# Performance work log

Hardware: AMD Instinct MI355X
Metric: run time of the kernel (lower is better)

The kernel has to match this reference:

```python
import jax, jax.numpy as jnp
import numpy as np

D = 64        # dense voxel grid extent per axis
C = 256       # planes
R = 128       # planes // reduction
N = 100000    # number of occupied (unique) sparse voxels
K = 7         # max-pool kernel size
PAD = 3       # (K-1)//2, stride-1 'same' window


def setup_inputs() -> dict:
    key = jax.random.key(0)
    k1, k2, k3, k4 = jax.random.split(key, 4)
    feats = jax.random.normal(k1, (N, C), dtype=jnp.float32)
    # unique sparse coordinates in [0, D)^3 (MinkowskiEngine coords are unique)
    lin = jax.random.permutation(k2, D * D * D)[:N]
    coords = jnp.stack(jnp.unravel_index(lin, (D, D, D)), axis=-1).astype(jnp.int32)
    # 1x1 sparse convs == per-point linear layers (ME default bias=False)
    W1 = jax.random.normal(k3, (C, R), dtype=jnp.float32) * (1.0 / np.sqrt(C))
    W2 = jax.random.normal(k4, (R, C), dtype=jnp.float32) * (1.0 / np.sqrt(R))
    return {"feats": feats, "coords": coords, "W1": W1, "W2": W2}


def reference(feats, coords, W1, W2):
    neg_inf = jnp.array(-jnp.inf, dtype=feats.dtype)
    ix, iy, iz = coords[:, 0], coords[:, 1], coords[:, 2]
    # scatter sparse features into a dense grid; empty voxels = -inf so they
    grid = jnp.full((D, D, D, C), neg_inf, dtype=feats.dtype).at[ix, iy, iz].set(feats)
    # MinkowskiMaxPooling(kernel_size=7, stride=1): max over [-3,3]^3 window
    pooled = jax.lax.reduce_window(
        grid, neg_inf, jax.lax.max,
        window_dimensions=(K, K, K, 1),
        window_strides=(1, 1, 1, 1),
        padding=[(PAD, PAD), (PAD, PAD), (PAD, PAD), (0, 0)],
    )
    y = pooled[ix, iy, iz]  # [N, C], gather back to sparse points
    # fc: 1x1 conv -> ReLU -> 1x1 conv -> sigmoid (per-point MLP)
    y = jax.nn.sigmoid(jax.nn.relu(y @ W1) @ W2)
    return feats * y
```

## Files before the change

kernel.cpp:

```cpp
#include <hip/hip_runtime.h>
#include <hip/hip_bf16.h>

#define GD 64
#define GC 256

typedef unsigned short u16;
typedef unsigned int u32;
typedef short bf16x8 __attribute__((ext_vector_type(8)));
typedef float f32x4 __attribute__((ext_vector_type(4)));

__device__ __forceinline__ u16 f2bf_rne(float f) {
    u32 u = __builtin_bit_cast(u32, f);
    u = (u + 0x7FFFu + ((u >> 16) & 1u)) >> 16;
    return (u16)u;
}

__device__ __forceinline__ float bfval(float f) {
    u32 u = __builtin_bit_cast(u32, f);
    u = (u + 0x7FFFu + ((u >> 16) & 1u)) & 0xFFFF0000u;
    return __builtin_bit_cast(float, u);
}

__device__ __forceinline__ void unpack8(uint4 r, float* w) {
    u32 v[4] = {r.x, r.y, r.z, r.w};
#pragma unroll
    for (int i = 0; i < 4; i++) {
        w[2 * i]     = __builtin_bit_cast(float, v[i] << 16);
        w[2 * i + 1] = __builtin_bit_cast(float, v[i] & 0xFFFF0000u);
    }
}

__global__ __launch_bounds__(256) void init_map(uint4* __restrict__ m) {
    int i = blockIdx.x * 256 + threadIdx.x;
    uint4 v;
    v.x = v.y = v.z = v.w = 0xFFFFFFFFu;
    m[i] = v;
}

__global__ __launch_bounds__(256) void build_map(const int* __restrict__ coords,
        int* __restrict__ map, int n) {
    int i = blockIdx.x * 256 + threadIdx.x;
    if (i < n) {
        int ix = coords[3 * i], iy = coords[3 * i + 1], iz = coords[3 * i + 2];
        map[(ix * GD + iy) * GD + iz] = i;
    }
}

__global__ __launch_bounds__(256) void pool_z_gather(const float* __restrict__ feats,
        const int* __restrict__ map, u16* __restrict__ grid) {
    int chunk = threadIdx.x & 31;
    int L = blockIdx.x * 8 + (threadIdx.x >> 5);
    const int* mrow = map + L * GD;
    u16* p = grid + (size_t)L * GD * GC + chunk * 8;

    float win[7][8];
#pragma unroll
    for (int s = 0; s < 7; s++)
#pragma unroll
        for (int cc = 0; cc < 8; cc++) win[s][cc] = -INFINITY;

#pragma unroll
    for (int t = 0; t < 3; t++) {
        int mi = mrow[t];
        if (mi >= 0) {
            const float4* f4 = (const float4*)(feats + (size_t)mi * GC + chunk * 8);
            float4 a = f4[0], b = f4[1];
            win[t + 3][0] = bfval(a.x); win[t + 3][1] = bfval(a.y);
            win[t + 3][2] = bfval(a.z); win[t + 3][3] = bfval(a.w);
            win[t + 3][4] = bfval(b.x); win[t + 3][5] = bfval(b.y);
            win[t + 3][6] = bfval(b.z); win[t + 3][7] = bfval(b.w);
        }
    }

#pragma unroll
    for (int z = 0; z < 64; z++) {
        int slot = (z + 6) % 7;
        bool live = false;
        if (z + 3 < 64) {
            int mi = mrow[z + 3];
            if (mi >= 0) {
                live = true;
                const float4* f4 = (const float4*)(feats + (size_t)mi * GC + chunk * 8);
                float4 a = f4[0], b = f4[1];
                win[slot][0] = bfval(a.x); win[slot][1] = bfval(a.y);
                win[slot][2] = bfval(a.z); win[slot][3] = bfval(a.w);
                win[slot][4] = bfval(b.x); win[slot][5] = bfval(b.y);
                win[slot][6] = bfval(b.z); win[slot][7] = bfval(b.w);
            }
        }
        if (!live) {
#pragma unroll
            for (int cc = 0; cc < 8; cc++) win[slot][cc] = -INFINITY;
        }
        u32 q[4];
#pragma unroll
        for (int i = 0; i < 4; i++) {
            u32 halves[2];
#pragma unroll
            for (int hh = 0; hh < 2; hh++) {
                int c = 2 * i + hh;
                float m01 = fmaxf(win[0][c], win[1][c]);
                float m23 = fmaxf(win[2][c], win[3][c]);
                float m45 = fmaxf(win[4][c], win[5][c]);
                float m = fmaxf(fmaxf(m01, m23), fmaxf(m45, win[6][c]));
                halves[hh] = __builtin_bit_cast(u32, m);
            }
            q[i] = (halves[0] >> 16) | (halves[1] & 0xFFFF0000u);
        }
        *(uint4*)(p + (size_t)z * GC) = make_uint4(q[0], q[1], q[2], q[3]);
    }
}

__global__ __launch_bounds__(256) void pool_pass_v(u16* __restrict__ grid,
        int mulA, int mulB, int strideCell) {
    int chunk = threadIdx.x & 31;
    int L = blockIdx.x * 8 + (threadIdx.x >> 5);
    int a = L >> 6, b = L & 63;
    size_t baseEl = ((size_t)a * mulA + (size_t)b * mulB) * GC + chunk * 8;
    size_t stepEl = (size_t)strideCell * GC;
    u16* p = grid + baseEl;

    float win[7][8];
#pragma unroll
    for (int s = 0; s < 7; s++)
#pragma unroll
        for (int c = 0; c < 8; c++) win[s][c] = -INFINITY;

#pragma unroll
    for (int t = 0; t < 3; t++) {
        uint4 r = *(const uint4*)(p + (size_t)t * stepEl);
        unpack8(r, win[t + 3]);
    }

#pragma unroll
    for (int z = 0; z < 64; z++) {
        int slot = (z + 6) % 7;
        if (z + 3 < 64) {
            uint4 r = *(const uint4*)(p + (size_t)(z + 3) * stepEl);
            unpack8(r, win[slot]);
        } else {
#pragma unroll
            for (int c = 0; c < 8; c++) win[slot][c] = -INFINITY;
        }
        u32 q[4];
#pragma unroll
        for (int i = 0; i < 4; i++) {
            u32 halves[2];
#pragma unroll
            for (int hh = 0; hh < 2; hh++) {
                int c = 2 * i + hh;
                float m01 = fmaxf(win[0][c], win[1][c]);
                float m23 = fmaxf(win[2][c], win[3][c]);
                float m45 = fmaxf(win[4][c], win[5][c]);
                float m = fmaxf(fmaxf(m01, m23), fmaxf(m45, win[6][c]));
                halves[hh] = __builtin_bit_cast(u32, m);
            }
            q[i] = (halves[0] >> 16) | (halves[1] & 0xFFFF0000u);
        }
        *(uint4*)(p + (size_t)z * stepEl) = make_uint4(q[0], q[1], q[2], q[3]);
    }
}

__global__ __launch_bounds__(256) void pool_x_compact(const u16* __restrict__ grid,
        const int* __restrict__ map, u16* __restrict__ P) {
    int chunk = threadIdx.x & 31;
    int L = blockIdx.x * 8 + (threadIdx.x >> 5);
    int cellBase = L;
    const u16* p = grid + (size_t)cellBase * GC + chunk * 8;
    size_t stepEl = (size_t)(GD * GD) * GC;

    float win[7][8];
#pragma unroll
    for (int s = 0; s < 7; s++)
#pragma unroll
        for (int cc = 0; cc < 8; cc++) win[s][cc] = -INFINITY;

#pragma unroll
    for (int t = 0; t < 3; t++) {
        uint4 r = *(const uint4*)(p + (size_t)t * stepEl);
        unpack8(r, win[t + 3]);
    }

#pragma unroll
    for (int x = 0; x < 64; x++) {
        int slot = (x + 6) % 7;
        if (x + 3 < 64) {
            uint4 r = *(const uint4*)(p + (size_t)(x + 3) * stepEl);
            unpack8(r, win[slot]);
        } else {
#pragma unroll
            for (int cc = 0; cc < 8; cc++) win[slot][cc] = -INFINITY;
        }
        int mi = map[cellBase + x * GD * GD];
        if (mi >= 0) {
            u32 q[4];
#pragma unroll
            for (int iq = 0; iq < 4; iq++) {
                u32 halves[2];
#pragma unroll
                for (int hh = 0; hh < 2; hh++) {
                    int cc = 2 * iq + hh;
                    float m01 = fmaxf(win[0][cc], win[1][cc]);
                    float m23 = fmaxf(win[2][cc], win[3][cc]);
                    float m45 = fmaxf(win[4][cc], win[5][cc]);
                    float m = fmaxf(fmaxf(m01, m23), fmaxf(m45, win[6][cc]));
                    halves[hh] = __builtin_bit_cast(u32, m);
                }
                q[iq] = (halves[0] >> 16) | (halves[1] & 0xFFFF0000u);
            }
            *(uint4*)(P + (size_t)mi * GC + chunk * 8) = make_uint4(q[0], q[1], q[2], q[3]);
        }
    }
}

__global__ __launch_bounds__(256) void prep_weights(const float* __restrict__ W1,
        const float* __restrict__ W2, u16* __restrict__ img1, u16* __restrict__ img2) {
    int t = blockIdx.x * 256 + threadIdx.x;
    if (t < 32768) {
        int h = t >> 14, nn = (t >> 8) & 63, chunk = (t >> 3) & 31, j = t & 7;
        int k = chunk * 8 + j;
        img1[(h << 14) + nn * 256 + (((chunk ^ (nn & 7)) << 3) | j)] =
            f2bf_rne(W1[k * 128 + h * 64 + nn]);
    } else {
        int t2 = t - 32768;
        int h = t2 >> 14, nn = (t2 >> 7) & 127, chunk = (t2 >> 3) & 15, j = t2 & 7;
        int k = chunk * 8 + j;
        img2[(h << 14) + nn * 128 + (((chunk ^ (nn & 7)) << 3) | j)] =
            f2bf_rne(W2[k * 256 + h * 128 + nn]);
    }
}

__global__ __launch_bounds__(256, 4) void gemm1_kernel(const u16* __restrict__ P,
        const u16* __restrict__ img1, u16* __restrict__ H, int n, int nrb) {
    __shared__ __align__(16) u16 w1t[64 * 256];
    int h = blockIdx.x >= nrb;
    int rb = blockIdx.x - (h ? nrb : 0);
    int tid = threadIdx.x;

    const uint4* src = (const uint4*)(img1 + (h << 14));
    uint4* dst = (uint4*)w1t;
#pragma unroll
    for (int i = 0; i < 8; i++) dst[i * 256 + tid] = src[i * 256 + tid];

    int wave = tid >> 6, lane = tid & 63, m16 = lane & 15, quad = lane >> 4;
    int row_a = rb * 64 + wave * 16 + m16;
    int ra = min(row_a, n - 1);
    const u16* yrow = P + (size_t)ra * GC;
    bf16x8 afr[8];
#pragma unroll
    for (int kk = 0; kk < 8; kk++)
        afr[kk] = *(const bf16x8*)(yrow + kk * 32 + quad * 8);
    __syncthreads();

    f32x4 acc[4];
#pragma unroll
    for (int t = 0; t < 4; t++) acc[t] = (f32x4){0.f, 0.f, 0.f, 0.f};
#pragma unroll
    for (int kk = 0; kk < 8; kk++) {
        int chunk = kk * 4 + quad;
#pragma unroll
        for (int t = 0; t < 4; t++) {
            int r = t * 16 + m16;
            bf16x8 b = *(const bf16x8*)&w1t[r * 256 + ((chunk ^ (r & 7)) << 3)];
            acc[t] = __builtin_amdgcn_mfma_f32_16x16x32_bf16(afr[kk], b, acc[t], 0, 0, 0);
        }
    }
    __syncthreads();

    u16* hbuf = w1t;
#pragma unroll
    for (int t = 0; t < 4; t++) {
        int col = t * 16 + m16;
        int c8 = col >> 3, j = col & 7;
#pragma unroll
        for (int rr = 0; rr < 4; rr++) {
            int row_l = wave * 16 + quad * 4 + rr;
            float hv = fmaxf(acc[t][rr], 0.0f);
            hbuf[row_l * 64 + (((c8 ^ (row_l & 7)) << 3) | j)] = f2bf_rne(hv);
        }
    }
    __syncthreads();
#pragma unroll
    for (int i = 0; i < 2; i++) {
        int cid = i * 256 + tid;
        int row_l = cid >> 3, c8 = cid & 7;
        int grow = rb * 64 + row_l;
        if (grow < n) {
            bf16x8 v = *(const bf16x8*)&hbuf[row_l * 64 + ((c8 ^ (row_l & 7)) << 3)];
            *(bf16x8*)&H[(size_t)grow * 128 + h * 64 + c8 * 8] = v;
        }
    }
}

__global__ __launch_bounds__(256, 4) void gemm2_kernel(const u16* __restrict__ H,
        const u16* __restrict__ img2, const float* __restrict__ feats,
        float* __restrict__ out, int n, int nrb) {
    __shared__ __align__(16) char smem[64 * 140 * 4];
    u16* w2t = (u16*)smem;
    float* zbuf = (float*)smem;
    int h = blockIdx.x >= nrb;
    int rb = blockIdx.x - (h ? nrb : 0);
    int tid = threadIdx.x;

    const uint4* src = (const uint4*)(img2 + (h << 14));
    uint4* dst = (uint4*)w2t;
#pragma unroll
    for (int i = 0; i < 8; i++) dst[i * 256 + tid] = src[i * 256 + tid];

    int wave = tid >> 6, lane = tid & 63, m16 = lane & 15, quad = lane >> 4;
    int row_a = rb * 64 + wave * 16 + m16;
    int ra = min(row_a, n - 1);
    const u16* hrow = H + (size_t)ra * 128;
    bf16x8 afr[4];
#pragma unroll
    for (int kk = 0; kk < 4; kk++)
        afr[kk] = *(const bf16x8*)(hrow + kk * 32 + quad * 8);
    __syncthreads();

    f32x4 acc[8];
#pragma unroll
    for (int t = 0; t < 8; t++) acc[t] = (f32x4){0.f, 0.f, 0.f, 0.f};
#pragma unroll
    for (int kk = 0; kk < 4; kk++) {
        int chunk = kk * 4 + quad;
#pragma unroll
        for (int t = 0; t < 8; t++) {
            int nn = t * 16 + m16;
            bf16x8 b = *(const bf16x8*)&w2t[nn * 128 + ((chunk ^ (nn & 7)) << 3)];
            acc[t] = __builtin_amdgcn_mfma_f32_16x16x32_bf16(afr[kk], b, acc[t], 0, 0, 0);
        }
    }
    __syncthreads();

#pragma unroll
    for (int t = 0; t < 8; t++) {
        int col = t * 16 + m16;
#pragma unroll
        for (int rr = 0; rr < 4; rr++) {
            int row_l = wave * 16 + quad * 4 + rr;
            zbuf[row_l * 140 + col] = acc[t][rr];
        }
    }
    __syncthreads();
#pragma unroll
    for (int i = 0; i < 8; i++) {
        int f = i * 256 + tid;
        int row_l = f >> 5, c4 = f & 31;
        int grow = rb * 64 + row_l;
        if (grow < n) {
            f32x4 z = *(const f32x4*)&zbuf[row_l * 140 + c4 * 4];
            size_t o = (size_t)grow * 256 + h * 128 + c4 * 4;
            f32x4 ft = *(const f32x4*)&feats[o];
            f32x4 r;
#pragma unroll
            for (int c = 0; c < 4; c++)
                r[c] = ft[c] / (1.0f + __expf(-z[c]));
            *(f32x4*)&out[o] = r;
        }
    }
}

extern "C" void kernel_launch(void* const* d_in, const int* in_sizes, int n_in,
                              void* d_out, int out_size, void* d_ws, size_t ws_size,
                              hipStream_t stream) {
    const float* feats = (const float*)d_in[0];
    const int* coords = (const int*)d_in[1];
    const float* W1 = (const float*)d_in[2];
    const float* W2 = (const float*)d_in[3];
    float* out = (float*)d_out;

    int n = in_sizes[1] / 3;

    size_t grid_bytes = (size_t)GD * GD * GD * GC * 2;
    size_t P_bytes = (size_t)n * GC * 2;
    size_t H_bytes = (size_t)n * 128 * 2;
    u16* grid = (u16*)d_ws;
    u16* P = (u16*)((char*)d_ws + grid_bytes);
    u16* H = (u16*)((char*)d_ws + grid_bytes + P_bytes);
    int* map = (int*)((char*)d_ws + grid_bytes + P_bytes + H_bytes);
    u16* img1 = (u16*)((char*)map + (size_t)GD * GD * GD * 4);
    u16* img2 = img1 + 32768;

    init_map<<<256, 256, 0, stream>>>((uint4*)map);
    prep_weights<<<256, 256, 0, stream>>>(W1, W2, img1, img2);
    build_map<<<(n + 255) / 256, 256, 0, stream>>>(coords, map, n);

    pool_z_gather<<<512, 256, 0, stream>>>(feats, map, grid);
    pool_pass_v<<<512, 256, 0, stream>>>(grid, GD * GD, 1, GD);
    pool_x_compact<<<512, 256, 0, stream>>>(grid, map, P);

    int nrb = (n + 63) / 64;
    gemm1_kernel<<<2 * nrb, 256, 0, stream>>>(P, img1, H, n, nrb);
    gemm2_kernel<<<2 * nrb, 256, 0, stream>>>(H, img2, feats, out, n, nrb);
}
```

Measured before the change: 448.2 us.

## Split pooling lines into halves and ping-pong the y pass between grids

Each separable max-pool pass now splits every 64-long line into two 32-output halves handled by separate warps, with a 6-element halo reload. This doubles the number of blocks to raise occupancy and latency hiding. Map indices are loaded once per warp and broadcast with shuffles instead of per-iteration scalar loads. The y pass now writes to a second grid buffer instead of working in place, which avoids read/write hazards between halves but doubles workspace and adds halo re-read traffic.

Result: faster. 375.1 us (-16.3%).

```diff
diff --git a/kernel.cpp b/kernel.cpp
--- a/kernel.cpp
+++ b/kernel.cpp
@@ -28,6 +28,25 @@
         w[2 * i]     = __builtin_bit_cast(float, v[i] << 16);
         w[2 * i + 1] = __builtin_bit_cast(float, v[i] & 0xFFFF0000u);
     }
+}
+
+__device__ __forceinline__ uint4 maxpack(const float (&win)[7][8]) {
+    u32 q[4];
+#pragma unroll
+    for (int i = 0; i < 4; i++) {
+        u32 halves[2];
+#pragma unroll
+        for (int hh = 0; hh < 2; hh++) {
+            int c = 2 * i + hh;
+            float m01 = fmaxf(win[0][c], win[1][c]);
+            float m23 = fmaxf(win[2][c], win[3][c]);
+            float m45 = fmaxf(win[4][c], win[5][c]);
+            float m = fmaxf(fmaxf(m01, m23), fmaxf(m45, win[6][c]));
+            halves[hh] = __builtin_bit_cast(u32, m);
+        }
+        q[i] = (halves[0] >> 16) | (halves[1] & 0xFFFF0000u);
+    }
+    return make_uint4(q[0], q[1], q[2], q[3]);
 }
 
 __global__ __launch_bounds__(256) void init_map(uint4* __restrict__ m) {
@@ -46,171 +65,156 @@
     }
 }
 
+template<int Z0>
+__device__ __forceinline__ void pool_z_half(const float* __restrict__ fb,
+        int2 mv, u16* __restrict__ p) {
+    float win[7][8];
+#pragma unroll
+    for (int s = 0; s < 7; s++)
+#pragma unroll
+        for (int c = 0; c < 8; c++) win[s][c] = -INFINITY;
+
+#pragma unroll
+    for (int t = 0; t < 6; t++) {
+        const int w = Z0 - 3 + t;
+        if (w >= 0) {
+            int mi = __shfl((w & 1) ? mv.y : mv.x, (w >> 1) & 31, 32);
+            if (mi >= 0) {
+                const float4* f4 = (const float4*)(fb + (size_t)mi * GC);
+                float4 a = f4[0], b = f4[1];
+                float* ws = win[(w + 3) % 7];
+                ws[0] = bfval(a.x); ws[1] = bfval(a.y);
+                ws[2] = bfval(a.z); ws[3] = bfval(a.w);
+                ws[4] = bfval(b.x); ws[5] = bfval(b.y);
+                ws[6] = bfval(b.z); ws[7] = bfval(b.w);
+            }
+        }
+    }
+
+#pragma unroll
+    for (int d = 0; d < 32; d++) {
+        const int z = Z0 + d, w = z + 3, slot = (w + 3) % 7;
+        bool live = false;
+        if (w < 64) {
+            int mi = __shfl((w & 1) ? mv.y : mv.x, (w >> 1) & 31, 32);
+            if (mi >= 0) {
+                live = true;
+                const float4* f4 = (const float4*)(fb + (size_t)mi * GC);
+                float4 a = f4[0], b = f4[1];
+                float* ws = win[slot];
+                ws[0] = bfval(a.x); ws[1] = bfval(a.y);
+                ws[2] = bfval(a.z); ws[3] = bfval(a.w);
+                ws[4] = bfval(b.x); ws[5] = bfval(b.y);
+                ws[6] = bfval(b.z); ws[7] = bfval(b.w);
+            }
+        }
+        if (!live) {
+#pragma unroll
+            for (int c = 0; c < 8; c++) win[slot][c] = -INFINITY;
+        }
+        *(uint4*)(p + (size_t)z * GC) = maxpack(win);
+    }
+}
+
 __global__ __launch_bounds__(256) void pool_z_gather(const float* __restrict__ feats,
         const int* __restrict__ map, u16* __restrict__ grid) {
-    int chunk = threadIdx.x & 31;
-    int L = blockIdx.x * 8 + (threadIdx.x >> 5);
-    const int* mrow = map + L * GD;
-    u16* p = grid + (size_t)L * GD * GC + chunk * 8;
-
+    int lane = threadIdx.x & 31;
+    int g = blockIdx.x * 8 + (threadIdx.x >> 5);
+    int L = g & 4095;
+    int2 mv = ((const int2*)(map + L * GD))[lane];
+    const float* fb = feats + lane * 8;
+    u16* p = grid + (size_t)L * GD * GC + lane * 8;
+    if (g < 4096) pool_z_half<0>(fb, mv, p);
+    else          pool_z_half<32>(fb, mv, p);
+}
+
+template<int A0>
+__device__ __forceinline__ void pool_line_dense(const u16* __restrict__ ip,
+        u16* __restrict__ op, size_t stepEl) {
     float win[7][8];
 #pragma unroll
     for (int s = 0; s < 7; s++)
 #pragma unroll
-        for (int cc = 0; cc < 8; cc++) win[s][cc] = -INFINITY;
-
-#pragma unroll
-    for (int t = 0; t < 3; t++) {
-        int mi = mrow[t];
-        if (mi >= 0) {
-            const float4* f4 = (const float4*)(feats + (size_t)mi * GC + chunk * 8);
-            float4 a = f4[0], b = f4[1];
-            win[t + 3][0] = bfval(a.x); win[t + 3][1] = bfval(a.y);
-            win[t + 3][2] = bfval(a.z); win[t + 3][3] = bfval(a.w);
-            win[t + 3][4] = bfval(b.x); win[t + 3][5] = bfval(b.y);
-            win[t + 3][6] = bfval(b.z); win[t + 3][7] = bfval(b.w);
-        }
-    }
-
-#pragma unroll
-    for (int z = 0; z < 64; z++) {
-        int slot = (z + 6) % 7;
-        bool live = false;
-        if (z + 3 < 64) {
-            int mi = mrow[z + 3];
-            if (mi >= 0) {
-                live = true;
-                const float4* f4 = (const float4*)(feats + (size_t)mi * GC + chunk * 8);
-                float4 a = f4[0], b = f4[1];
-                win[slot][0] = bfval(a.x); win[slot][1] = bfval(a.y);
-                win[slot][2] = bfval(a.z); win[slot][3] = bfval(a.w);
-                win[slot][4] = bfval(b.x); win[slot][5] = bfval(b.y);
-                win[slot][6] = bfval(b.z); win[slot][7] = bfval(b.w);
-            }
-        }
-        if (!live) {
-#pragma unroll
-            for (int cc = 0; cc < 8; cc++) win[slot][cc] = -INFINITY;
-        }
-        u32 q[4];
-#pragma unroll
-        for (int i = 0; i < 4; i++) {
-            u32 halves[2];
-#pragma unroll
-            for (int hh = 0; hh < 2; hh++) {
-                int c = 2 * i + hh;
-                float m01 = fmaxf(win[0][c], win[1][c]);
-                float m23 = fmaxf(win[2][c], win[3][c]);
-                float m45 = fmaxf(win[4][c], win[5][c]);
-                float m = fmaxf(fmaxf(m01, m23), fmaxf(m45, win[6][c]));
-                halves[hh] = __builtin_bit_cast(u32, m);
-            }
-            q[i] = (halves[0] >> 16) | (halves[1] & 0xFFFF0000u);
-        }
-        *(uint4*)(p + (size_t)z * GC) = make_uint4(q[0], q[1], q[2], q[3]);
-    }
-}
-
-__global__ __launch_bounds__(256) void pool_pass_v(u16* __restrict__ grid,
-        int mulA, int mulB, int strideCell) {
-    int chunk = threadIdx.x & 31;
-    int L = blockIdx.x * 8 + (threadIdx.x >> 5);
-    int a = L >> 6, b = L & 63;
-    size_t baseEl = ((size_t)a * mulA + (size_t)b * mulB) * GC + chunk * 8;
-    size_t stepEl = (size_t)strideCell * GC;
-    u16* p = grid + baseEl;
-
-    float win[7][8];
-#pragma unroll
-    for (int s = 0; s < 7; s++)
-#pragma unroll
         for (int c = 0; c < 8; c++) win[s][c] = -INFINITY;
 
 #pragma unroll
-    for (int t = 0; t < 3; t++) {
-        uint4 r = *(const uint4*)(p + (size_t)t * stepEl);
-        unpack8(r, win[t + 3]);
-    }
-
-#pragma unroll
-    for (int z = 0; z < 64; z++) {
-        int slot = (z + 6) % 7;
-        if (z + 3 < 64) {
-            uint4 r = *(const uint4*)(p + (size_t)(z + 3) * stepEl);
+    for (int t = 0; t < 6; t++) {
+        const int w = A0 - 3 + t;
+        if (w >= 0) {
+            uint4 r = *(const uint4*)(ip + (size_t)w * stepEl);
+            unpack8(r, win[(w + 3) % 7]);
+        }
+    }
+#pragma unroll
+    for (int d = 0; d < 32; d++) {
+        const int a = A0 + d, w = a + 3, slot = (w + 3) % 7;
+        if (w < 64) {
+            uint4 r = *(const uint4*)(ip + (size_t)w * stepEl);
             unpack8(r, win[slot]);
         } else {
 #pragma unroll
             for (int c = 0; c < 8; c++) win[slot][c] = -INFINITY;
         }
-        u32 q[4];
-#pragma unroll
-        for (int i = 0; i < 4; i++) {
-            u32 halves[2];
-#pragma unroll
-            for (int hh = 0; hh < 2; hh++) {
-                int c = 2 * i + hh;
-                float m01 = fmaxf(win[0][c], win[1][c]);
-                float m23 = fmaxf(win[2][c], win[3][c]);
-                float m45 = fmaxf(win[4][c], win[5][c]);
-                float m = fmaxf(fmaxf(m01, m23), fmaxf(m45, win[6][c]));
-                halves[hh] = __builtin_bit_cast(u32, m);
-            }
-            q[i] = (halves[0] >> 16) | (halves[1] & 0xFFFF0000u);
-        }
-        *(uint4*)(p + (size_t)z * stepEl) = make_uint4(q[0], q[1], q[2], q[3]);
-    }
-}
-
-__global__ __launch_bounds__(256) void pool_x_compact(const u16* __restrict__ grid,
-        const int* __restrict__ map, u16* __restrict__ P) {
-    int chunk = threadIdx.x & 31;
-    int L = blockIdx.x * 8 + (threadIdx.x >> 5);
-    int cellBase = L;
-    const u16* p = grid + (size_t)cellBase * GC + chunk * 8;
-    size_t stepEl = (size_t)(GD * GD) * GC;
-
+        *(uint4*)(op + (size_t)a * stepEl) = maxpack(win);
+    }
+}
+
+__global__ __launch_bounds__(256) void pool_y(const u16* __restrict__ gin,
+        u16* __restrict__ gout) {
+    int lane = threadIdx.x & 31;
+    int g = blockIdx.x * 8 + (threadIdx.x >> 5);
+    int L = g & 4095;
+    int x = L >> 6, z = L & 63;
+    size_t base = ((size_t)x * GD * GD + z) * GC + lane * 8;
+    size_t stepEl = (size_t)GD * GC;
+    if (g < 4096) pool_line_dense<0>(gin + base, gout + base, stepEl);
+    else          pool_line_dense<32>(gin + base, gout + base, stepEl);
+}
+
+template<int X0>
+__device__ __forceinline__ void pool_x_half(const u16* __restrict__ ip, size_t stepEl,
+        int m0, int m1, u16* __restrict__ P, int chunkoff) {
     float win[7][8];
 #pragma unroll
     for (int s = 0; s < 7; s++)
 #pragma unroll
-        for (int cc = 0; cc < 8; cc++) win[s][cc] = -INFINITY;
-
-#pragma unroll
-    for (int t = 0; t < 3; t++) {
-        uint4 r = *(const uint4*)(p + (size_t)t * stepEl);
-        unpack8(r, win[t + 3]);
-    }
-
-#pragma unroll
-    for (int x = 0; x < 64; x++) {
-        int slot = (x + 6) % 7;
-        if (x + 3 < 64) {
-            uint4 r = *(const uint4*)(p + (size_t)(x + 3) * stepEl);
+        for (int c = 0; c < 8; c++) win[s][c] = -INFINITY;
+
+#pragma unroll
+    for (int t = 0; t < 6; t++) {
+        const int w = X0 - 3 + t;
+        if (w >= 0) {
+            uint4 r = *(const uint4*)(ip + (size_t)w * stepEl);
+            unpack8(r, win[(w + 3) % 7]);
+        }
+    }
+#pragma unroll
+    for (int d = 0; d < 32; d++) {
+        const int a = X0 + d, w = a + 3, slot = (w + 3) % 7;
+        if (w < 64) {
+            uint4 r = *(const uint4*)(ip + (size_t)w * stepEl);
             unpack8(r, win[slot]);
         } else {
 #pragma unroll
-            for (int cc = 0; cc < 8; cc++) win[slot][cc] = -INFINITY;
-        }
-        int mi = map[cellBase + x * GD * GD];
-        if (mi >= 0) {
-            u32 q[4];
-#pragma unroll
-            for (int iq = 0; iq < 4; iq++) {
-                u32 halves[2];
-#pragma unroll
-                for (int hh = 0; hh < 2; hh++) {
-                    int cc = 2 * iq + hh;
-                    float m01 = fmaxf(win[0][cc], win[1][cc]);
-                    float m23 = fmaxf(win[2][cc], win[3][cc]);
-                    float m45 = fmaxf(win[4][cc], win[5][cc]);
-                    float m = fmaxf(fmaxf(m01, m23), fmaxf(m45, win[6][cc]));
-                    halves[hh] = __builtin_bit_cast(u32, m);
-                }
-                q[iq] = (halves[0] >> 16) | (halves[1] & 0xFFFF0000u);
-            }
-            *(uint4*)(P + (size_t)mi * GC + chunk * 8) = make_uint4(q[0], q[1], q[2], q[3]);
-        }
-    }
+            for (int c = 0; c < 8; c++) win[slot][c] = -INFINITY;
+        }
+        int mi = __shfl((a < 32) ? m0 : m1, a & 31, 32);
+        if (mi >= 0)
+            *(uint4*)(P + (size_t)mi * GC + chunkoff) = maxpack(win);
+    }
+}
+
+__global__ __launch_bounds__(256) void pool_x_compact(const u16* __restrict__ gin,
+        const int* __restrict__ map, u16* __restrict__ P) {
+    int lane = threadIdx.x & 31;
+    int g = blockIdx.x * 8 + (threadIdx.x >> 5);
+    int L = g & 4095;
+    int m0 = map[L + lane * GD * GD];
+    int m1 = map[L + (lane + 32) * GD * GD];
+    size_t base = (size_t)L * GC + lane * 8;
+    size_t stepEl = (size_t)GD * GD * GC;
+    if (g < 4096) pool_x_half<0>(gin + base, stepEl, m0, m1, P, lane * 8);
+    else          pool_x_half<32>(gin + base, stepEl, m0, m1, P, lane * 8);
 }
 
 __global__ __launch_bounds__(256) void prep_weights(const float* __restrict__ W1,
@@ -375,9 +379,10 @@
     size_t P_bytes = (size_t)n * GC * 2;
     size_t H_bytes = (size_t)n * 128 * 2;
     u16* grid = (u16*)d_ws;
-    u16* P = (u16*)((char*)d_ws + grid_bytes);
-    u16* H = (u16*)((char*)d_ws + grid_bytes + P_bytes);
-    int* map = (int*)((char*)d_ws + grid_bytes + P_bytes + H_bytes);
+    u16* grid2 = (u16*)((char*)d_ws + grid_bytes);
+    u16* P = (u16*)((char*)d_ws + 2 * grid_bytes);
+    u16* H = (u16*)((char*)d_ws + 2 * grid_bytes + P_bytes);
+    int* map = (int*)((char*)d_ws + 2 * grid_bytes + P_bytes + H_bytes);
     u16* img1 = (u16*)((char*)map + (size_t)GD * GD * GD * 4);
     u16* img2 = img1 + 32768;
 
@@ -385,9 +390,9 @@
     prep_weights<<<256, 256, 0, stream>>>(W1, W2, img1, img2);
     build_map<<<(n + 255) / 256, 256, 0, stream>>>(coords, map, n);
 
-    pool_z_gather<<<512, 256, 0, stream>>>(feats, map, grid);
-    pool_pass_v<<<512, 256, 0, stream>>>(grid, GD * GD, 1, GD);
-    pool_x_compact<<<512, 256, 0, stream>>>(grid, map, P);
+    pool_z_gather<<<1024, 256, 0, stream>>>(feats, map, grid);
+    pool_y<<<1024, 256, 0, stream>>>(grid, grid2);
+    pool_x_compact<<<1024, 256, 0, stream>>>(grid2, map, P);
 
     int nrb = (n + 63) / 64;
     gemm1_kernel<<<2 * nrb, 256, 0, stream>>>(P, img1, H, n, nrb);
```
